# Performance work log

Hardware: AMD Instinct MI355X
Metric: run time of the kernel (lower is better)

## Reference

```python
import jax, jax.numpy as jnp
import numpy as np

ROI = 7   # roi_size
SR = 2    # sampling_ratio


def _interp_axis(t, size):
    # torchvision bilinear_interpolate semantics along one axis
    valid = (t > -1.0) & (t < size)
    t = jnp.clip(t, 0.0, None)
    low = jnp.minimum(jnp.floor(t).astype(jnp.int32), size - 1)
    high = jnp.minimum(low + 1, size - 1)
    t = jnp.where(low >= size - 1, low.astype(t.dtype), t)
    frac = t - low.astype(t.dtype)
    return valid, low, high, frac


def roi_align(fmap, boxes):
    """torchvision RoIAlign(output=(7,7), spatial_scale=1.0, sampling_ratio=2, aligned=False).
    fmap: [B,H,W,C] (channel-last; equivalent to torch's NCHW math), boxes: [N,5].
    Returns [N,C,ROI,ROI]."""
    B, H, W, C = fmap.shape
    N = boxes.shape[0]
    b = boxes[:, 0].astype(jnp.int32)
    x1, y1, x2, y2 = boxes[:, 1], boxes[:, 2], boxes[:, 3], boxes[:, 4]
    roi_w = jnp.maximum(x2 - x1, 1.0)
    roi_h = jnp.maximum(y2 - y1, 1.0)
    bin_w = roi_w / ROI
    bin_h = roi_h / ROI
    # per-bin sample offsets in bin units: (ph + (i+0.5)/SR) flattened over (bin, sample)
    grid = ((jnp.arange(ROI, dtype=fmap.dtype)[:, None] * SR
             + jnp.arange(SR, dtype=fmap.dtype)[None, :] + 0.5) / SR).reshape(-1)  # [ROI*SR]
    ys = y1[:, None] + grid[None, :] * bin_h[:, None]  # [N, S]
    xs = x1[:, None] + grid[None, :] * bin_w[:, None]  # [N, S]

    vy, yl, yh, ly = _interp_axis(ys, H)
    vx, xl, xh, lx = _interp_axis(xs, W)
    hy, hx = 1.0 - ly, 1.0 - lx

    bN = b[:, None, None]
    gather = lambda yi, xi: fmap[bN, yi[:, :, None], xi[:, None, :]]        # [N,S,S,C]
    wgt = lambda a, c: (a[:, :, None] * c[:, None, :])[..., None]           # [N,S,S,1]
    val = (wgt(hy, hx) * gather(yl, xl) + wgt(hy, lx) * gather(yl, xh)
           + wgt(ly, hx) * gather(yh, xl) + wgt(ly, lx) * gather(yh, xh))
    val = val * (vy[:, :, None] & vx[:, None, :])[..., None].astype(val.dtype)
    pooled = val.reshape(N, ROI, SR, ROI, SR, C).mean(axis=(2, 4))          # [N,ROI,ROI,C]
    return pooled.transpose(0, 3, 1, 2)                                     # [N,C,ROI,ROI]


def setup_inputs() -> dict:
    key = jax.random.key(0)
    kf, kb, kx1, kx2, ky1, ky2, kw1, kw2 = jax.random.split(key, 8)
    B, H, W, C = 8, 64, 64, 768
    N = 256
    feature_map = jax.random.normal(kf, (B, H, W, C), dtype=jnp.float32)
    bidx = jax.random.randint(kb, (N,), 0, B).astype(jnp.float32)
    x1 = jax.random.uniform(kx1, (N,)) * (W / 2)
    y1 = jax.random.uniform(ky1, (N,)) * (H / 2)
    x2 = x1 + 1.0 + jax.random.uniform(kx2, (N,)) * (W / 2 - 1.0)
    y2 = y1 + 1.0 + jax.random.uniform(ky2, (N,)) * (H / 2 - 1.0)
    lesion_bboxes = jnp.stack([bidx, x1, y1, x2, y2], axis=1).astype(jnp.float32)
    in_dim = C * ROI * ROI  # 37632
    W1 = jax.random.normal(kw1, (in_dim, 1024), dtype=jnp.float32) * 0.02
    b1 = jnp.zeros((1024,), dtype=jnp.float32)
    W2 = jax.random.normal(kw2, (1024, 512), dtype=jnp.float32) * 0.02
    b2 = jnp.zeros((512,), dtype=jnp.float32)
    return {"feature_map": feature_map, "lesion_bboxes": lesion_bboxes,
            "W1": W1, "b1": b1, "W2": W2, "b2": b2}


def reference(feature_map, lesion_bboxes, W1, b1, W2, b2):
    roi = roi_align(feature_map, lesion_bboxes)          # [N,C,7,7]
    flat = roi.reshape(roi.shape[0], -1)                  # channel-major flatten, as torch
    h = jax.nn.relu(flat @ W1 + b1)                       # Dropout(0.1) is identity in eval
    return h @ W2 + b2                                    # [N,512]
```

## Files before the change

### kernel.cpp

```cpp
#include <hip/hip_runtime.h>
#include <hip/hip_bf16.h>

typedef __attribute__((ext_vector_type(8))) short bfrag8;
typedef __attribute__((ext_vector_type(4))) float f32x4;

__device__ __forceinline__ unsigned short f2bf(float f) {
  unsigned int u = __float_as_uint(f);
  u += 0x7FFFu + ((u >> 16) & 1u);
  return (unsigned short)(u >> 16);
}

__device__ __forceinline__ void interp1(float t, int size, int& lo, int& hi, float& frac, bool& valid) {
  valid = (t > -1.0f) && (t < (float)size);
  t = fmaxf(t, 0.0f);
  lo = (int)t;
  if (lo > size - 1) lo = size - 1;
  hi = lo + 1; if (hi > size - 1) hi = size - 1;
  if (lo >= size - 1) t = (float)lo;
  frac = t - (float)lo;
}

__global__ __launch_bounds__(192) void roi_kernel(const float* __restrict__ fmap,
                                                  const float* __restrict__ boxes,
                                                  unsigned short* __restrict__ A) {
  const int ph = blockIdx.x;
  const int n  = blockIdx.y;
  const int t  = threadIdx.x;

  const float* bx = boxes + n * 5;
  const int b = (int)bx[0];
  const float x1 = bx[1], y1 = bx[2], x2 = bx[3], y2 = bx[4];
  const float bw = fmaxf(x2 - x1, 1.0f) * (1.0f / 7.0f);
  const float bh = fmaxf(y2 - y1, 1.0f) * (1.0f / 7.0f);

  const float* fb = fmap + (size_t)b * 64 * 64 * 768 + t * 4;

  int yl[2], yh[2]; float ly[2], hy[2]; bool vy[2];
  #pragma unroll
  for (int sy = 0; sy < 2; sy++) {
    float y = y1 + (ph * 2 + sy + 0.5f) * 0.5f * bh;
    interp1(y, 64, yl[sy], yh[sy], ly[sy], vy[sy]);
    hy[sy] = 1.0f - ly[sy];
  }

  float4 acc[7];
  #pragma unroll
  for (int pw = 0; pw < 7; pw++) acc[pw] = make_float4(0.f, 0.f, 0.f, 0.f);

  #pragma unroll
  for (int pw = 0; pw < 7; pw++) {
    #pragma unroll
    for (int sx = 0; sx < 2; sx++) {
      float x = x1 + (pw * 2 + sx + 0.5f) * 0.5f * bw;
      int xl, xh; float lx; bool vx;
      interp1(x, 64, xl, xh, lx, vx);
      float hx = 1.0f - lx;
      if (vx) {
        #pragma unroll
        for (int sy = 0; sy < 2; sy++) {
          if (vy[sy]) {
            float4 v00 = *(const float4*)(fb + (yl[sy] * 64 + xl) * 768);
            float4 v01 = *(const float4*)(fb + (yl[sy] * 64 + xh) * 768);
            float4 v10 = *(const float4*)(fb + (yh[sy] * 64 + xl) * 768);
            float4 v11 = *(const float4*)(fb + (yh[sy] * 64 + xh) * 768);
            float w00 = hy[sy] * hx, w01 = hy[sy] * lx, w10 = ly[sy] * hx, w11 = ly[sy] * lx;
            acc[pw].x += w00 * v00.x + w01 * v01.x + w10 * v10.x + w11 * v11.x;
            acc[pw].y += w00 * v00.y + w01 * v01.y + w10 * v10.y + w11 * v11.y;
            acc[pw].z += w00 * v00.z + w01 * v01.z + w10 * v10.z + w11 * v11.z;
            acc[pw].w += w00 * v00.w + w01 * v01.w + w10 * v10.w + w11 * v11.w;
          }
        }
      }
    }
  }

  unsigned short* arow = A + (size_t)n * 37632 + (size_t)(ph * 7) * 768 + t * 4;
  #pragma unroll
  for (int pw = 0; pw < 7; pw++) {
    float sx0 = acc[pw].x * 0.25f, sy0 = acc[pw].y * 0.25f;
    float sz0 = acc[pw].z * 0.25f, sw0 = acc[pw].w * 0.25f;
    uint2 pk;
    pk.x = (unsigned)f2bf(sx0) | ((unsigned)f2bf(sy0) << 16);
    pk.y = (unsigned)f2bf(sz0) | ((unsigned)f2bf(sw0) << 16);
    *(uint2*)(arow + (size_t)pw * 768) = pk;
  }
}

template<int KT, int NT, int STEPS, int NNT, bool PERM>
__global__ __launch_bounds__(256, 2) void gemm_splitk(const unsigned short* __restrict__ A,
                                                      const float* __restrict__ B,
                                                      float* __restrict__ part) {
  __shared__ unsigned short Al[2][256 * 64];
  __shared__ unsigned short Bl[2][64 * 64];

  const int nwg = gridDim.x;
  const int bid = blockIdx.x;
  const int work = (bid & 7) * (nwg >> 3) + (bid >> 3);
  const int ks = work / NNT;
  const int nt = work - ks * NNT;
  const int n0 = nt * 64;
  const int k0 = ks * (STEPS * 64);

  const int t = (int)threadIdx.x;
  const int lane = t & 63, wid = t >> 6;
  const int kp = t & 31;
  const int nq = t >> 5;

  f32x4 acc[4][4];
  #pragma unroll
  for (int i = 0; i < 4; i++)
    #pragma unroll
    for (int j = 0; j < 4; j++) acc[i][j] = (f32x4){0.f, 0.f, 0.f, 0.f};

  float4 b_a0, b_a1, b_c0, b_c1;

  auto issueA = [&](int buf, int s) {
    #pragma unroll
    for (int i = 0; i < 8; i++) {
      const int r0 = wid * 64 + i * 8;
      const int row = r0 + (lane >> 3);
      const int j = (lane & 7) ^ (row & 7);
      const unsigned short* g = A + (size_t)row * KT + (k0 + s * 64 + j * 8);
      __builtin_amdgcn_global_load_lds(
          (const __attribute__((address_space(1))) void*)g,
          (__attribute__((address_space(3))) void*)&Al[buf][r0 * 64],
          16, 0, 0);
    }
  };

  auto loadB = [&](int s) {
    int k = k0 + s * 64 + 2 * kp;
    int r0, dr;
    if (PERM) { int bin = k / 768; int c = k - bin * 768; r0 = c * 49 + bin; dr = 49; }
    else      { r0 = k; dr = 1; }
    const float* p0 = B + (size_t)r0 * NT + n0 + nq * 8;
    const float* p1 = p0 + (size_t)dr * NT;
    b_a0 = *(const float4*)(p0);
    b_a1 = *(const float4*)(p0 + 4);
    b_c0 = *(const float4*)(p1);
    b_c1 = *(const float4*)(p1 + 4);
  };

  auto writeB = [&](int buf) {
    char* base = (char*)&Bl[buf][0];
    const int klo = (kp & 3) * 4, kslot = kp >> 2;
    int nrow = nq * 8;
    #define WR_B(ii, fa, fc) { \
      int r = nrow + ii; \
      unsigned v = (unsigned)f2bf(fa) | ((unsigned)f2bf(fc) << 16); \
      *(unsigned*)(base + r * 128 + ((kslot ^ (r & 7)) << 4) + klo) = v; }
    WR_B(0, b_a0.x, b_c0.x) WR_B(1, b_a0.y, b_c0.y)
    WR_B(2, b_a0.z, b_c0.z) WR_B(3, b_a0.w, b_c0.w)
    WR_B(4, b_a1.x, b_c1.x) WR_B(5, b_a1.y, b_c1.y)
    WR_B(6, b_a1.z, b_c1.z) WR_B(7, b_a1.w, b_c1.w)
    #undef WR_B
  };

  auto compute = [&](int buf) {
    const char* abase = (const char*)&Al[buf][0];
    const char* bbase = (const char*)&Bl[buf][0];
    #pragma unroll
    for (int kk = 0; kk < 2; kk++) {
      const int slot = kk * 4 + (lane >> 4);
      bfrag8 af[4], bf[4];
      #pragma unroll
      for (int fm = 0; fm < 4; fm++) {
        const int r = wid * 64 + fm * 16 + (lane & 15);
        af[fm] = *(const bfrag8*)(abase + r * 128 + ((slot ^ (r & 7)) << 4));
      }
      #pragma unroll
      for (int fn = 0; fn < 4; fn++) {
        const int r = fn * 16 + (lane & 15);
        bf[fn] = *(const bfrag8*)(bbase + r * 128 + ((slot ^ (r & 7)) << 4));
      }
      #pragma unroll
      for (int fm = 0; fm < 4; fm++)
        #pragma unroll
        for (int fn = 0; fn < 4; fn++)
          acc[fm][fn] = __builtin_amdgcn_mfma_f32_16x16x32_bf16(af[fm], bf[fn], acc[fm][fn], 0, 0, 0);
    }
  };

  issueA(0, 0);
  loadB(0);
  writeB(0);
  __syncthreads();

  int buf = 0;
  for (int s = 0; s < STEPS; s++) {
    if (s + 1 < STEPS) {
      issueA(buf ^ 1, s + 1);
      loadB(s + 1);
    }
    compute(buf);
    if (s + 1 < STEPS) writeB(buf ^ 1);
    __syncthreads();
    buf ^= 1;
  }

  const int r4 = (lane >> 4) * 4, cn = lane & 15;
  #pragma unroll
  for (int fm = 0; fm < 4; fm++)
    #pragma unroll
    for (int fn = 0; fn < 4; fn++)
      #pragma unroll
      for (int q = 0; q < 4; q++) {
        int m = wid * 64 + fm * 16 + r4 + q;
        part[((size_t)ks * 256 + m) * NT + n0 + fn * 16 + cn] = acc[fm][fn][q];
      }
}

__global__ __launch_bounds__(256) void reduce_relu_28(const float* __restrict__ part,
                                                      const float* __restrict__ b1,
                                                      unsigned short* __restrict__ h) {
  const int i4 = blockIdx.x * 256 + threadIdx.x;
  const float4* p4 = (const float4*)part;
  float4 s = p4[i4];
  #pragma unroll
  for (int p = 1; p < 28; p++) {
    float4 v = p4[(size_t)p * 65536 + i4];
    s.x += v.x; s.y += v.y; s.z += v.z; s.w += v.w;
  }
  float4 bb = ((const float4*)b1)[i4 & 255];
  s.x = fmaxf(s.x + bb.x, 0.f); s.y = fmaxf(s.y + bb.y, 0.f);
  s.z = fmaxf(s.z + bb.z, 0.f); s.w = fmaxf(s.w + bb.w, 0.f);
  uint2 pk;
  pk.x = (unsigned)f2bf(s.x) | ((unsigned)f2bf(s.y) << 16);
  pk.y = (unsigned)f2bf(s.z) | ((unsigned)f2bf(s.w) << 16);
  ((uint2*)h)[i4] = pk;
}

__global__ __launch_bounds__(256) void reduce_bias_8(const float* __restrict__ part,
                                                     const float* __restrict__ b2,
                                                     float* __restrict__ out) {
  const int i4 = blockIdx.x * 256 + threadIdx.x;
  const float4* p4 = (const float4*)part;
  float4 s = p4[i4];
  #pragma unroll
  for (int p = 1; p < 8; p++) {
    float4 v = p4[(size_t)p * 32768 + i4];
    s.x += v.x; s.y += v.y; s.z += v.z; s.w += v.w;
  }
  float4 bb = ((const float4*)b2)[i4 & 127];
  s.x += bb.x; s.y += bb.y; s.z += bb.z; s.w += bb.w;
  ((float4*)out)[i4] = s;
}

extern "C" void kernel_launch(void* const* d_in, const int* in_sizes, int n_in,
                              void* d_out, int out_size, void* d_ws, size_t ws_size,
                              hipStream_t stream) {
  const float* fmap  = (const float*)d_in[0];
  const float* boxes = (const float*)d_in[1];
  const float* W1    = (const float*)d_in[2];
  const float* b1    = (const float*)d_in[3];
  const float* W2    = (const float*)d_in[4];
  const float* b2    = (const float*)d_in[5];
  float* out = (float*)d_out;

  char* ws = (char*)d_ws;
  unsigned short* Aroi = (unsigned short*)ws;
  float* part1 = (float*)(ws + 19267584);
  unsigned short* h = (unsigned short*)(ws + 19267584 + 29360128);
  float* part2 = (float*)(ws + 19267584 + 29360128 + 524288);

  roi_kernel<<<dim3(7, 256), 192, 0, stream>>>(fmap, boxes, Aroi);
  gemm_splitk<37632, 1024, 21, 16, true><<<448, 256, 0, stream>>>(Aroi, W1, part1);
  reduce_relu_28<<<256, 256, 0, stream>>>(part1, b1, h);
  gemm_splitk<1024, 512, 2, 8, false><<<64, 256, 0, stream>>>(h, W2, part2);
  reduce_bias_8<<<128, 256, 0, stream>>>(part2, b2, out);
}
```

Measured before the change: 350.0 us.

## Emit ROI features in channel-major order so W1 rows stream contiguously

The ROI kernel now gives each block one box and a quarter of the channels. It loops over all 49 bins, stages the bf16 results in shared memory in channel-major (c*49+bin) order, and writes them out contiguously. This matches torch's flatten order, so the first GEMM can read W1 rows sequentially instead of through a permuted, strided gather. The B-tile load and the LDS swizzle are rearranged to fit. In exchange the ROI gather becomes scalar per channel and runs serially over bins, with fewer but longer blocks.

```diff
diff --git a/kernel.cpp b/kernel.cpp
--- a/kernel.cpp
+++ b/kernel.cpp
@@ -23,9 +23,10 @@
 __global__ __launch_bounds__(192) void roi_kernel(const float* __restrict__ fmap,
                                                   const float* __restrict__ boxes,
                                                   unsigned short* __restrict__ A) {
-  const int ph = blockIdx.x;
-  const int n  = blockIdx.y;
-  const int t  = threadIdx.x;
+  const int bid = blockIdx.x;
+  const int n = bid >> 2, q = bid & 3;
+  const int t = threadIdx.x;
+  __shared__ unsigned short T[192 * 49];
 
   const float* bx = boxes + n * 5;
   const int b = (int)bx[0];
@@ -33,60 +34,53 @@
   const float bw = fmaxf(x2 - x1, 1.0f) * (1.0f / 7.0f);
   const float bh = fmaxf(y2 - y1, 1.0f) * (1.0f / 7.0f);
 
-  const float* fb = fmap + (size_t)b * 64 * 64 * 768 + t * 4;
-
-  int yl[2], yh[2]; float ly[2], hy[2]; bool vy[2];
-  #pragma unroll
-  for (int sy = 0; sy < 2; sy++) {
-    float y = y1 + (ph * 2 + sy + 0.5f) * 0.5f * bh;
-    interp1(y, 64, yl[sy], yh[sy], ly[sy], vy[sy]);
-    hy[sy] = 1.0f - ly[sy];
-  }
-
-  float4 acc[7];
-  #pragma unroll
-  for (int pw = 0; pw < 7; pw++) acc[pw] = make_float4(0.f, 0.f, 0.f, 0.f);
-
-  #pragma unroll
-  for (int pw = 0; pw < 7; pw++) {
-    #pragma unroll
-    for (int sx = 0; sx < 2; sx++) {
-      float x = x1 + (pw * 2 + sx + 0.5f) * 0.5f * bw;
-      int xl, xh; float lx; bool vx;
-      interp1(x, 64, xl, xh, lx, vx);
-      float hx = 1.0f - lx;
-      if (vx) {
-        #pragma unroll
-        for (int sy = 0; sy < 2; sy++) {
-          if (vy[sy]) {
-            float4 v00 = *(const float4*)(fb + (yl[sy] * 64 + xl) * 768);
-            float4 v01 = *(const float4*)(fb + (yl[sy] * 64 + xh) * 768);
-            float4 v10 = *(const float4*)(fb + (yh[sy] * 64 + xl) * 768);
-            float4 v11 = *(const float4*)(fb + (yh[sy] * 64 + xh) * 768);
-            float w00 = hy[sy] * hx, w01 = hy[sy] * lx, w10 = ly[sy] * hx, w11 = ly[sy] * lx;
-            acc[pw].x += w00 * v00.x + w01 * v01.x + w10 * v10.x + w11 * v11.x;
-            acc[pw].y += w00 * v00.y + w01 * v01.y + w10 * v10.y + w11 * v11.y;
-            acc[pw].z += w00 * v00.z + w01 * v01.z + w10 * v10.z + w11 * v11.z;
-            acc[pw].w += w00 * v00.w + w01 * v01.w + w10 * v10.w + w11 * v11.w;
+  const int c = q * 192 + t;
+  const float* fb = fmap + (size_t)b * 64 * 64 * 768 + c;
+
+  for (int ph = 0; ph < 7; ph++) {
+    int yl[2], yh[2]; float ly[2], hy[2]; bool vy[2];
+    #pragma unroll
+    for (int sy = 0; sy < 2; sy++) {
+      float y = y1 + (ph * 2 + sy + 0.5f) * 0.5f * bh;
+      interp1(y, 64, yl[sy], yh[sy], ly[sy], vy[sy]);
+      hy[sy] = 1.0f - ly[sy];
+    }
+    float acc[7];
+    #pragma unroll
+    for (int pw = 0; pw < 7; pw++) acc[pw] = 0.0f;
+
+    #pragma unroll
+    for (int pw = 0; pw < 7; pw++) {
+      #pragma unroll
+      for (int sx = 0; sx < 2; sx++) {
+        float x = x1 + (pw * 2 + sx + 0.5f) * 0.5f * bw;
+        int xl, xh; float lx; bool vx;
+        interp1(x, 64, xl, xh, lx, vx);
+        float hx = 1.0f - lx;
+        if (vx) {
+          #pragma unroll
+          for (int sy = 0; sy < 2; sy++) {
+            if (vy[sy]) {
+              float v00 = fb[(yl[sy] * 64 + xl) * 768];
+              float v01 = fb[(yl[sy] * 64 + xh) * 768];
+              float v10 = fb[(yh[sy] * 64 + xl) * 768];
+              float v11 = fb[(yh[sy] * 64 + xh) * 768];
+              acc[pw] += hy[sy] * (hx * v00 + lx * v01) + ly[sy] * (hx * v10 + lx * v11);
+            }
           }
         }
       }
-    }
-  }
-
-  unsigned short* arow = A + (size_t)n * 37632 + (size_t)(ph * 7) * 768 + t * 4;
-  #pragma unroll
-  for (int pw = 0; pw < 7; pw++) {
-    float sx0 = acc[pw].x * 0.25f, sy0 = acc[pw].y * 0.25f;
-    float sz0 = acc[pw].z * 0.25f, sw0 = acc[pw].w * 0.25f;
-    uint2 pk;
-    pk.x = (unsigned)f2bf(sx0) | ((unsigned)f2bf(sy0) << 16);
-    pk.y = (unsigned)f2bf(sz0) | ((unsigned)f2bf(sw0) << 16);
-    *(uint2*)(arow + (size_t)pw * 768) = pk;
-  }
-}
-
-template<int KT, int NT, int STEPS, int NNT, bool PERM>
+      T[t * 49 + ph * 7 + pw] = f2bf(acc[pw] * 0.25f);
+    }
+  }
+  __syncthreads();
+  const unsigned* Ts = (const unsigned*)T;
+  unsigned* out = (unsigned*)(A + (size_t)n * 37632 + q * 9408);
+  #pragma unroll 4
+  for (int i = t; i < 4704; i += 192) out[i] = Ts[i];
+}
+
+template<int KT, int NT, int STEPS, int NNT>
 __global__ __launch_bounds__(256, 2) void gemm_splitk(const unsigned short* __restrict__ A,
                                                       const float* __restrict__ B,
                                                       float* __restrict__ part) {
@@ -103,8 +97,6 @@
 
   const int t = (int)threadIdx.x;
   const int lane = t & 63, wid = t >> 6;
-  const int kp = t & 31;
-  const int nq = t >> 5;
 
   f32x4 acc[4][4];
   #pragma unroll
@@ -112,7 +104,7 @@
     #pragma unroll
     for (int j = 0; j < 4; j++) acc[i][j] = (f32x4){0.f, 0.f, 0.f, 0.f};
 
-  float4 b_a0, b_a1, b_c0, b_c1;
+  float4 b00, b01, b10, b11;
 
   auto issueA = [&](int buf, int s) {
     #pragma unroll
@@ -129,31 +121,27 @@
   };
 
   auto loadB = [&](int s) {
-    int k = k0 + s * 64 + 2 * kp;
-    int r0, dr;
-    if (PERM) { int bin = k / 768; int c = k - bin * 768; r0 = c * 49 + bin; dr = 49; }
-    else      { r0 = k; dr = 1; }
-    const float* p0 = B + (size_t)r0 * NT + n0 + nq * 8;
-    const float* p1 = p0 + (size_t)dr * NT;
-    b_a0 = *(const float4*)(p0);
-    b_a1 = *(const float4*)(p0 + 4);
-    b_c0 = *(const float4*)(p1);
-    b_c1 = *(const float4*)(p1 + 4);
+    const float* p = B + (size_t)(k0 + s * 64 + (t >> 4) * 2) * NT + n0 + (t & 15) * 4;
+    b00 = *(const float4*)p;
+    b01 = *(const float4*)(p + NT);
+    b10 = *(const float4*)(p + 32 * (size_t)NT);
+    b11 = *(const float4*)(p + 33 * (size_t)NT);
   };
 
   auto writeB = [&](int buf) {
     char* base = (char*)&Bl[buf][0];
-    const int klo = (kp & 3) * 4, kslot = kp >> 2;
-    int nrow = nq * 8;
-    #define WR_B(ii, fa, fc) { \
-      int r = nrow + ii; \
-      unsigned v = (unsigned)f2bf(fa) | ((unsigned)f2bf(fc) << 16); \
-      *(unsigned*)(base + r * 128 + ((kslot ^ (r & 7)) << 4) + klo) = v; }
-    WR_B(0, b_a0.x, b_c0.x) WR_B(1, b_a0.y, b_c0.y)
-    WR_B(2, b_a0.z, b_c0.z) WR_B(3, b_a0.w, b_c0.w)
-    WR_B(4, b_a1.x, b_c1.x) WR_B(5, b_a1.y, b_c1.y)
-    WR_B(6, b_a1.z, b_c1.z) WR_B(7, b_a1.w, b_c1.w)
-    #undef WR_B
+    const int lo = ((t >> 4) & 3) * 4;
+    const int nb = (t & 15) * 4;
+    #define WRB(g, j, fa, fb_) { \
+      int nn = nb + j; \
+      int slot = (g) * 4 + wid; \
+      unsigned v = (unsigned)f2bf(fa) | ((unsigned)f2bf(fb_) << 16); \
+      *(unsigned*)(base + nn * 128 + ((slot ^ ((nn >> 3) & 7)) << 4) + lo) = v; }
+    WRB(0, 0, b00.x, b01.x) WRB(0, 1, b00.y, b01.y)
+    WRB(0, 2, b00.z, b01.z) WRB(0, 3, b00.w, b01.w)
+    WRB(1, 0, b10.x, b11.x) WRB(1, 1, b10.y, b11.y)
+    WRB(1, 2, b10.z, b11.z) WRB(1, 3, b10.w, b11.w)
+    #undef WRB
   };
 
   auto compute = [&](int buf) {
@@ -171,7 +159,7 @@
       #pragma unroll
       for (int fn = 0; fn < 4; fn++) {
         const int r = fn * 16 + (lane & 15);
-        bf[fn] = *(const bfrag8*)(bbase + r * 128 + ((slot ^ (r & 7)) << 4));
+        bf[fn] = *(const bfrag8*)(bbase + r * 128 + ((slot ^ ((r >> 3) & 7)) << 4));
       }
       #pragma unroll
       for (int fm = 0; fm < 4; fm++)
@@ -263,9 +251,9 @@
   unsigned short* h = (unsigned short*)(ws + 19267584 + 29360128);
   float* part2 = (float*)(ws + 19267584 + 29360128 + 524288);
 
-  roi_kernel<<<dim3(7, 256), 192, 0, stream>>>(fmap, boxes, Aroi);
-  gemm_splitk<37632, 1024, 21, 16, true><<<448, 256, 0, stream>>>(Aroi, W1, part1);
+  roi_kernel<<<1024, 192, 0, stream>>>(fmap, boxes, Aroi);
+  gemm_splitk<37632, 1024, 21, 16><<<448, 256, 0, stream>>>(Aroi, W1, part1);
   reduce_relu_28<<<256, 256, 0, stream>>>(part1, b1, h);
-  gemm_splitk<1024, 512, 2, 8, false><<<64, 256, 0, stream>>>(h, W2, part2);
+  gemm_splitk<1024, 512, 2, 8><<<64, 256, 0, stream>>>(h, W2, part2);
   reduce_bias_8<<<128, 256, 0, stream>>>(part2, b2, out);
 }
```

Measured after the change: 399.2 us. +14.0%, slower.
